# Performance work log

Measured on AMD Instinct MI355X. Metric: run time of the kernel, lower is better.

The kernel has to match this reference:

```python
import jax, jax.numpy as jnp
import numpy as np

B, N, G, K, C = 16, 8192, 128, 32, 384
EPS = 1e-5


def _fps(xyz, n):
    # furthest point sampling starting at index 0 (matches pointnet2 CUDA op)
    b = xyz.shape[0]
    dists = jnp.sum((xyz - xyz[:, :1]) ** 2, -1)  # [B,N] dist^2 to first pt

    def step(d, _):
        idx = jnp.argmax(d, axis=-1)                       # [B]
        p = jnp.take_along_axis(xyz, idx[:, None, None], 1)  # [B,1,3]
        d = jnp.minimum(d, jnp.sum((xyz - p) ** 2, -1))
        return d, idx.astype(jnp.int32)

    _, idxs = jax.lax.scan(step, dists, None, length=n - 1)
    idx = jnp.concatenate([jnp.zeros((1, b), jnp.int32), idxs], 0).T  # [B,n]
    return jnp.take_along_axis(xyz, idx[..., None], axis=1)


def _morton_order(center):
    # greedy nearest-neighbour tour over group centers (simplied_morton_sorting)
    b, g, _ = center.shape
    d = jnp.sum((center[:, :, None] - center[:, None]) ** 2, -1)  # [B,G,G]
    d = jnp.where(jnp.eye(g, dtype=bool), jnp.inf, d)

    def step(carry, _):
        cur, visited = carry
        row = jnp.take_along_axis(d, cur[:, None, None], 1)[:, 0]  # [B,G]
        row = jnp.where(visited, jnp.inf, row)
        nxt = jnp.argmin(row, -1).astype(jnp.int32)
        visited = visited | jax.nn.one_hot(nxt, g, dtype=bool)
        return (nxt, visited), nxt

    cur0 = jnp.zeros((b,), jnp.int32)
    init = (cur0, jax.nn.one_hot(cur0, g, dtype=bool))
    _, nxts = jax.lax.scan(step, init, None, length=g - 1)
    return jnp.concatenate([jnp.zeros((1, b), jnp.int32), nxts], 0).T  # [B,G]


def _bn(x, g_, b_, m_, v_):
    return (x - m_) * (g_ * jax.lax.rsqrt(v_ + EPS)) + b_


def _pos_embed(center):
    npf = 128  # 384 // 3 // 2 * 2
    i = jnp.arange(npf, dtype=jnp.float32)
    dim_t = 10000.0 ** (2.0 * jnp.floor(i / 2) / npf)
    x = center * (2.0 * np.pi)
    pd = x[..., None] / dim_t                                # [B,G,3,128]
    emb = jnp.stack([jnp.sin(pd[..., 0::2]), jnp.cos(pd[..., 1::2])], -1)
    return emb.reshape(*center.shape[:-1], -1)               # [B,G,384]


def _forward(xyz, w1, b1, g1, bt1, m1, v1, w2, b2, w3, b3, g3, bt3, m3, v3, w4, b4):
    center = _fps(xyz, G)                                    # [B,G,3]
    # squared-distance KNN (argsort order identical to euclidean cdist)
    d2 = (jnp.sum(center ** 2, -1)[:, :, None]
          + jnp.sum(xyz ** 2, -1)[:, None]
          - 2.0 * jnp.einsum('bgd,bnd->bgn', center, xyz))   # [B,G,N]
    _, idx = jax.lax.top_k(-d2, K)                           # [B,G,K]
    neigh = jnp.take_along_axis(xyz, idx.reshape(B, G * K)[..., None], 1)
    neigh = neigh.reshape(B, G, K, 3) - center[:, :, None]
    order = _morton_order(center)                            # [B,G]
    neigh = jnp.take_along_axis(neigh, order[:, :, None, None], 1)
    center = jnp.take_along_axis(center, order[:, :, None], 1)
    # Encoder_small (1x1 convs == per-point linears, eval-mode BN)
    pg = neigh.reshape(B * G, K, 3)
    f = jax.nn.relu(_bn(pg @ w1.T + b1, g1, bt1, m1, v1)) @ w2.T + b2  # [BG,K,256]
    fg = jnp.max(f, 1, keepdims=True)
    h = jnp.concatenate([jnp.broadcast_to(fg, f.shape), f], -1)        # [BG,K,512]
    h = jax.nn.relu(_bn(h @ w3.T + b3, g3, bt3, m3, v3)) @ w4.T + b4   # [BG,K,384]
    tokens = jnp.max(h, 1).reshape(B, G, C)
    return tokens + _pos_embed(center)


def setup_inputs() -> dict:
    key = jax.random.key(0)
    ks = jax.random.split(key, 8)
    s = 0.05
    return {
        'xyz': jax.random.normal(ks[0], (B, N, 3), jnp.float32),
        'w1': jax.random.normal(ks[1], (128, 3), jnp.float32) * s,
        'b1': jax.random.normal(ks[2], (128,), jnp.float32) * s,
        'g1': jnp.ones((128,), jnp.float32),
        'bt1': jnp.zeros((128,), jnp.float32),
        'm1': jnp.zeros((128,), jnp.float32),
        'v1': jnp.ones((128,), jnp.float32),
        'w2': jax.random.normal(ks[3], (256, 128), jnp.float32) * s,
        'b2': jax.random.normal(ks[4], (256,), jnp.float32) * s,
        'w3': jax.random.normal(ks[5], (512, 512), jnp.float32) * s,
        'b3': jnp.zeros((512,), jnp.float32),
        'g3': jnp.ones((512,), jnp.float32),
        'bt3': jnp.zeros((512,), jnp.float32),
        'm3': jnp.zeros((512,), jnp.float32),
        'v3': jnp.ones((512,), jnp.float32),
        'w4': jax.random.normal(ks[6], (384, 512), jnp.float32) * s,
        'b4': jax.random.normal(ks[7], (384,), jnp.float32) * s,
    }


def reference(xyz, w1, b1, g1, bt1, m1, v1, w2, b2, w3, b3, g3, bt3, m3, v3, w4, b4):
    return _forward(xyz, w1, b1, g1, bt1, m1, v1, w2, b2, w3, b3, g3, bt3, m3, v3, w4, b4)
```

## Files before the change

### kernel.cpp

```cpp
#include <hip/hip_runtime.h>
#include <hip/hip_bf16.h>

#define B_ 16
#define N_ 8192
#define G_ 128
#define K_ 32
#define C_ 384
#define EPSV 1e-5f

typedef __attribute__((ext_vector_type(8))) short bf16x8;
typedef __attribute__((ext_vector_type(8))) unsigned short u16x8;
typedef __attribute__((ext_vector_type(4))) float f32x4;
typedef __attribute__((ext_vector_type(2))) float f32x2;

__device__ __forceinline__ unsigned short f2b(float f){
  unsigned int u = __float_as_uint(f);
  u += 0x7fffu + ((u >> 16) & 1u);
  return (unsigned short)(u >> 16);
}
__device__ __forceinline__ float b2f(unsigned short s){
  return __uint_as_float(((unsigned int)s) << 16);
}
__device__ __forceinline__ float sq3(float dx, float dy, float dz){
  return __fadd_rn(__fadd_rn(__fmul_rn(dx,dx), __fmul_rn(dy,dy)), __fmul_rn(dz,dz));
}
__device__ __forceinline__ f32x2 pkmax(f32x2 a, f32x2 b){
  return f32x2{fmaxf(a.x,b.x), fmaxf(a.y,b.y)};
}
__device__ __forceinline__ unsigned fenc(float f){
  unsigned u = __float_as_uint(f);
  return ((int)u >= 0) ? (u | 0x80000000u) : ~u;
}

#define DPP_MAXU_STAGE(r, CTRL) { \
  unsigned _o = (unsigned)__builtin_amdgcn_update_dpp((int)(r), (int)(r), (CTRL), 0xf, 0xf, false); \
  (r) = ((r) > _o) ? (r) : _o; }
#define DPP_MAXU_ALL(r) \
  DPP_MAXU_STAGE(r, 0x111) DPP_MAXU_STAGE(r, 0x112) DPP_MAXU_STAGE(r, 0x114) \
  DPP_MAXU_STAGE(r, 0x118) DPP_MAXU_STAGE(r, 0x142) DPP_MAXU_STAGE(r, 0x143)
#define DPP_MINU_STAGE(r, CTRL) { \
  unsigned _o = (unsigned)__builtin_amdgcn_update_dpp((int)(r), (int)(r), (CTRL), 0xf, 0xf, false); \
  (r) = ((r) < _o) ? (r) : _o; }
#define DPP_MINU_ALL(r) \
  DPP_MINU_STAGE(r, 0x111) DPP_MINU_STAGE(r, 0x112) DPP_MINU_STAGE(r, 0x114) \
  DPP_MINU_STAGE(r, 0x118) DPP_MINU_STAGE(r, 0x142) DPP_MINU_STAGE(r, 0x143)

__global__ __launch_bounds__(256) void prep_kernel(
    const float* __restrict__ w2, const float* __restrict__ w3,
    const float* __restrict__ w4, unsigned short* __restrict__ w2b,
    unsigned short* __restrict__ w3b, unsigned short* __restrict__ w4b){
  int i = blockIdx.x*256 + threadIdx.x;
  if (i < 32768){ w2b[i] = f2b(w2[i]); return; }
  i -= 32768;
  if (i < 262144){ w3b[i] = f2b(w3[i]); return; }
  i -= 262144;
  if (i < 196608){ w4b[i] = f2b(w4[i]); }
}

__attribute__((amdgpu_flat_work_group_size(256,256), amdgpu_waves_per_eu(1,1)))
__global__ void fps_morton_kernel(const float* __restrict__ xyz,
                                  float* __restrict__ centers_ord){
  const int b = blockIdx.x, t = threadIdx.x, w = t >> 6;
  const int lane = t & 63;
  const float* xb = xyz + (size_t)b*N_*3;
  __shared__ __align__(16) float sval[2][4];
  __shared__ __align__(16) int   sidx[2][4];
  __shared__ float clx[G_], cly[G_], clz[G_];
  const int base = t*32;
  f32x2 X[16], Y[16], Z[16], D[16];
  const float p0x = xb[0], p0y = xb[1], p0z = xb[2];
  {
#pragma clang fp contract(off)
    float s[96];
    const float4* src = (const float4*)(xb + (size_t)base*3);
    #pragma unroll
    for (int q = 0; q < 24; q++) ((float4*)s)[q] = src[q];
    #pragma unroll
    for (int p = 0; p < 16; p++){
      X[p] = f32x2{s[6*p+0], s[6*p+3]};
      Y[p] = f32x2{s[6*p+1], s[6*p+4]};
      Z[p] = f32x2{s[6*p+2], s[6*p+5]};
      const f32x2 dx = X[p] - p0x, dy = Y[p] - p0y, dz = Z[p] - p0z;
      D[p] = (dx*dx + dy*dy) + dz*dz;
    }
  }
  if (t == 0){ clx[0] = p0x; cly[0] = p0y; clz[0] = p0z; }
  int buf = 0;
  for (int g = 1; g < G_; g++){
    const f32x2 mm = pkmax(pkmax(pkmax(pkmax(D[0],D[1]),pkmax(D[2],D[3])),
                                 pkmax(pkmax(D[4],D[5]),pkmax(D[6],D[7]))),
                           pkmax(pkmax(pkmax(D[8],D[9]),pkmax(D[10],D[11])),
                                 pkmax(pkmax(D[12],D[13]),pkmax(D[14],D[15]))));
    const float v = fmaxf(mm.x, mm.y);
    int jl = 0;
    #pragma unroll
    for (int p = 15; p >= 0; p--){
      if (D[p].y == v) jl = 2*p+1;
      if (D[p].x == v) jl = 2*p;
    }
    const unsigned uv = __float_as_uint(v);
    unsigned r = uv;
    DPP_MAXU_ALL(r)
    const unsigned wmax = (unsigned)__builtin_amdgcn_readlane((int)r, 63);
    const unsigned long long tie = __ballot(uv == wmax);
    const int wl = __ffsll(tie) - 1;
    if (lane == wl){ sval[buf][w] = __uint_as_float(wmax); sidx[buf][w] = base + jl; }
    __syncthreads();
    const float4 vv = *(const float4*)&sval[buf][0];
    const int4   ii = *(const int4*)&sidx[buf][0];
    float bv = vv.x; int bb = ii.x;
    if (vv.y > bv){ bv = vv.y; bb = ii.y; }
    if (vv.z > bv){ bv = vv.z; bb = ii.z; }
    if (vv.w > bv){ bv = vv.w; bb = ii.w; }
    {
#pragma clang fp contract(off)
      const int ubb = __builtin_amdgcn_readfirstlane(bb);
      const float cx = xb[ubb*3], cy = xb[ubb*3+1], cz = xb[ubb*3+2];
      if (t == 0){ clx[g] = cx; cly[g] = cy; clz[g] = cz; }
      #pragma unroll
      for (int p = 0; p < 16; p++){
        const f32x2 dx = X[p] - cx, dy = Y[p] - cy, dz = Z[p] - cz;
        const f32x2 dn = (dx*dx + dy*dy) + dz*dz;
        D[p] = f32x2{fminf(D[p].x, dn.x), fminf(D[p].y, dn.y)};
      }
    }
    buf ^= 1;
  }
  __syncthreads();
  if (t < 64){
    float mcx[2], mcy[2], mcz[2]; bool mvis[2];
    #pragma unroll
    for (int j = 0; j < 2; j++){
      const int idx = lane + j*64;
      mcx[j] = clx[idx]; mcy[j] = cly[idx]; mcz[j] = clz[idx];
      mvis[j] = (idx == 0);
    }
    float curx = clx[0], cury = cly[0], curz = clz[0];
    if (lane == 0){
      centers_ord[(size_t)b*G_*3 + 0] = curx;
      centers_ord[(size_t)b*G_*3 + 1] = cury;
      centers_ord[(size_t)b*G_*3 + 2] = curz;
    }
    for (int step = 1; step < G_; step++){
      const float d0r = sq3(__fsub_rn(mcx[0],curx), __fsub_rn(mcy[0],cury), __fsub_rn(mcz[0],curz));
      const float d1r = sq3(__fsub_rn(mcx[1],curx), __fsub_rn(mcy[1],cury), __fsub_rn(mcz[1],curz));
      const float d0 = mvis[0] ? __builtin_inff() : d0r;
      const float d1 = mvis[1] ? __builtin_inff() : d1r;
      float mv = d0; int mi = lane;
      if (d1 < mv){ mv = d1; mi = lane + 64; }
      const int wj = mi >> 6;
      const float sx = wj ? mcx[1] : mcx[0];
      const float sy = wj ? mcy[1] : mcy[0];
      const float sz = wj ? mcz[1] : mcz[0];
      const unsigned key = __float_as_uint(mv);
      unsigned r = key;
      DPP_MINU_ALL(r)
      const unsigned wmin = (unsigned)__builtin_amdgcn_readlane((int)r, 63);
      const unsigned long long tie = __ballot(key == wmin);
      int wl;
      if (__popcll(tie) == 1){
        wl = __ffsll(tie) - 1;
      } else {
        float tv = mv; int ti = mi;
        #pragma unroll
        for (int mk = 1; mk < 64; mk <<= 1){
          const float ov = __shfl_xor(tv, mk);
          const int   oi = __shfl_xor(ti, mk);
          if (ov < tv || (ov == tv && oi < ti)){ tv = ov; ti = oi; }
        }
        wl = ti & 63;
      }
      const int mbi = __builtin_amdgcn_readlane(mi, wl);
      curx = __uint_as_float((unsigned)__builtin_amdgcn_readlane((int)__float_as_uint(sx), wl));
      cury = __uint_as_float((unsigned)__builtin_amdgcn_readlane((int)__float_as_uint(sy), wl));
      curz = __uint_as_float((unsigned)__builtin_amdgcn_readlane((int)__float_as_uint(sz), wl));
      if (lane == wl){
        if ((mbi >> 6) == 0) mvis[0] = true; else mvis[1] = true;
      }
      if (lane == 0){
        centers_ord[((size_t)b*G_ + step)*3 + 0] = curx;
        centers_ord[((size_t)b*G_ + step)*3 + 1] = cury;
        centers_ord[((size_t)b*G_ + step)*3 + 2] = curz;
      }
    }
  }
}

__global__ __launch_bounds__(256, 2) void knn_kernel(const float* __restrict__ xyz,
                                                     const float* __restrict__ centers_ord,
                                                     float* __restrict__ neigh){
  const int gp = blockIdx.x, b = blockIdx.y, t = threadIdx.x;
  const int lane = t & 63, w = t >> 6;
  __shared__ __align__(16) float sv[2][4];
  __shared__ __align__(16) int   si[2][4];
  __shared__ int list[K_];
  const float* xb = xyz + (size_t)b*N_*3;
  const float* cp = centers_ord + ((size_t)b*G_ + gp)*3;
  const float cxv = cp[0], cyv = cp[1], czv = cp[2];
  const float cc = sq3(cxv, cyv, czv);
  const int base = t*32;
  float dd[32];
  float v = __builtin_inff(); int jl = 0;
  {
    float s[96];
    const float4* src = (const float4*)(xb + (size_t)base*3);
    #pragma unroll
    for (int q = 0; q < 24; q++) ((float4*)s)[q] = src[q];
    #pragma unroll
    for (int j = 0; j < 32; j++){
      const float x = s[3*j], y = s[3*j+1], z = s[3*j+2];
      const float xx = sq3(x, y, z);
      const float dot = __fadd_rn(__fadd_rn(__fmul_rn(cxv,x), __fmul_rn(cyv,y)), __fmul_rn(czv,z));
      dd[j] = __fsub_rn(__fadd_rn(cc, xx), __fmul_rn(2.f, dot));
      if (dd[j] < v){ v = dd[j]; jl = j; }
    }
  }
  int buf = 0;
  for (int it = 0; it < K_; it++){
    const unsigned key = fenc(v);
    unsigned r = key;
    DPP_MINU_ALL(r)
    const unsigned wmin = (unsigned)__builtin_amdgcn_readlane((int)r, 63);
    const unsigned long long tie = __ballot(key == wmin);
    const int wl = __ffsll(tie) - 1;
    if (lane == wl){ sv[buf][w] = v; si[buf][w] = base + jl; }
    __syncthreads();
    const float4 vv = *(const float4*)&sv[buf][0];
    const int4   ii = *(const int4*)&si[buf][0];
    float bv = vv.x; int bb = ii.x;
    if (vv.y < bv){ bv = vv.y; bb = ii.y; }
    if (vv.z < bv){ bv = vv.z; bb = ii.z; }
    if (vv.w < bv){ bv = vv.w; bb = ii.w; }
    if (t == 0) list[it] = bb;
    if ((bb >> 5) == t){
      const int jw = bb & 31;
      #pragma unroll
      for (int j = 0; j < 32; j++) if (j == jw) dd[j] = __builtin_inff();
      v = __builtin_inff(); jl = 0;
      #pragma unroll
      for (int j = 0; j < 32; j++) if (dd[j] < v){ v = dd[j]; jl = j; }
    }
    buf ^= 1;
  }
  __syncthreads();
  if (t < K_*3){
    const int k = t / 3, d = t % 3;
    const int n = list[k];
    neigh[(((size_t)b*G_ + gp)*K_ + k)*3 + d] = __fsub_rn(xb[n*3+d], cp[d]);
  }
}

__device__ __forceinline__ int swzA1(int row, int col){
  int byteo = row*256 + col*2;
  byteo ^= (row & 7) << 4;
  return byteo >> 1;
}
__device__ __forceinline__ int swzF(int row, int col){
  int byteo = row*512 + col*2;
  byteo ^= (row & 7) << 4;
  return byteo >> 1;
}
__device__ __forceinline__ int swzA(int row, int col){
  int byteo = row*1024 + col*2;
  byteo ^= (row & 7) << 4;
  return byteo >> 1;
}

__global__ __launch_bounds__(512, 2) void enc_kernel(
    const float* __restrict__ neigh, const float* __restrict__ centers_ord,
    const float* __restrict__ w1, const float* __restrict__ b1,
    const float* __restrict__ g1, const float* __restrict__ bt1,
    const float* __restrict__ m1, const float* __restrict__ v1,
    const unsigned short* __restrict__ w2b, const float* __restrict__ b2,
    const unsigned short* __restrict__ w3b, const float* __restrict__ b3,
    const float* __restrict__ g3, const float* __restrict__ bt3,
    const float* __restrict__ m3, const float* __restrict__ v3,
    const unsigned short* __restrict__ w4b, const float* __restrict__ b4,
    float* __restrict__ out)
{
  const int t = threadIdx.x;
  const int lane = t & 63, w = t >> 6, lr = lane & 15, lg = lane >> 4;
  const int gid0 = blockIdx.x*2;
  __shared__ __align__(16) unsigned short A1s[2][32*128];
  __shared__ __align__(16) unsigned short Fl[2][32*256];
  __shared__ __align__(16) unsigned short A3s[2][32*512];
  __shared__ __align__(16) unsigned short fgb[2][256];
  float* tokp = (float*)&Fl[0][0];

  {
    const int g = t >> 8, rem = t & 255, p = rem >> 3, c0 = (rem & 7) * 16;
    const float* pgp = neigh + (size_t)(gid0 + g)*96 + p*3;
    const float px = pgp[0], py = pgp[1], pz = pgp[2];
    unsigned short hv[16];
    #pragma unroll
    for (int cc = 0; cc < 16; cc++){
      const int c = c0 + cc;
      const float wx = w1[c*3], wy = w1[c*3+1], wz = w1[c*3+2];
      const float sc = g1[c] * rsqrtf(v1[c] + EPSV);
      float val = px*wx + py*wy + pz*wz + b1[c];
      val = (val - m1[c])*sc + bt1[c];
      hv[cc] = f2b(fmaxf(val, 0.f));
    }
    *(u16x8*)&A1s[g][swzA1(p, c0)]     = *(u16x8*)&hv[0];
    *(u16x8*)&A1s[g][swzA1(p, c0 + 8)] = *(u16x8*)&hv[8];
  }
  __syncthreads();

  {
    const int col0 = w*32;
    f32x4 acc[2][2][2];
    #pragma unroll
    for (int nt = 0; nt < 2; nt++)
      #pragma unroll
      for (int g = 0; g < 2; g++)
        #pragma unroll
        for (int m = 0; m < 2; m++){ f32x4 z = {0.f,0.f,0.f,0.f}; acc[nt][g][m] = z; }
    #pragma unroll
    for (int kt = 0; kt < 4; kt++){
      bf16x8 bA[2][2];
      #pragma unroll
      for (int g = 0; g < 2; g++)
        #pragma unroll
        for (int m = 0; m < 2; m++)
          bA[g][m] = *(const bf16x8*)&A1s[g][swzA1(m*16 + lr, kt*32 + lg*8)];
      bf16x8 bB[2];
      #pragma unroll
      for (int nt = 0; nt < 2; nt++)
        bB[nt] = *(const bf16x8*)(w2b + (size_t)(col0 + nt*16 + lr)*128 + kt*32 + lg*8);
      #pragma unroll
      for (int nt = 0; nt < 2; nt++)
        #pragma unroll
        for (int g = 0; g < 2; g++)
          #pragma unroll
          for (int m = 0; m < 2; m++)
            acc[nt][g][m] = __builtin_amdgcn_mfma_f32_16x16x32_bf16(bA[g][m], bB[nt], acc[nt][g][m], 0,0,0);
    }
    #pragma unroll
    for (int nt = 0; nt < 2; nt++){
      const int col = col0 + nt*16 + lr;
      const float bc = b2[col];
      #pragma unroll
      for (int g = 0; g < 2; g++)
        #pragma unroll
        for (int m = 0; m < 2; m++)
          #pragma unroll
          for (int r = 0; r < 4; r++)
            Fl[g][swzF(m*16 + lg*4 + r, col)] = f2b(acc[nt][g][m][r] + bc);
    }
  }
  __syncthreads();

  {
    const int g = t >> 8, col = t & 255;
    float mx = -__builtin_inff();
    #pragma unroll 4
    for (int row = 0; row < 32; row++) mx = fmaxf(mx, b2f(Fl[g][swzF(row, col)]));
    fgb[g][col] = f2b(mx);
  }
  __syncthreads();

  {
    const int col0 = w*64;
    f32x4 acc[4][2][2];
    #pragma unroll
    for (int nt = 0; nt < 4; nt++)
      #pragma unroll
      for (int g = 0; g < 2; g++)
        #pragma unroll
        for (int m = 0; m < 2; m++){ f32x4 z = {0.f,0.f,0.f,0.f}; acc[nt][g][m] = z; }
    #pragma unroll
    for (int kt = 0; kt < 16; kt++){
      bf16x8 bA[2][2];
      if (kt < 8){
        #pragma unroll
        for (int g = 0; g < 2; g++){
          const bf16x8 af = *(const bf16x8*)&fgb[g][kt*32 + lg*8];
          bA[g][0] = af; bA[g][1] = af;
        }
      } else {
        #pragma unroll
        for (int g = 0; g < 2; g++)
          #pragma unroll
          for (int m = 0; m < 2; m++)
            bA[g][m] = *(const bf16x8*)&Fl[g][swzF(m*16 + lr, (kt-8)*32 + lg*8)];
      }
      bf16x8 bB[4];
      #pragma unroll
      for (int nt = 0; nt < 4; nt++)
        bB[nt] = *(const bf16x8*)(w3b + (size_t)(col0 + nt*16 + lr)*512 + kt*32 + lg*8);
      #pragma unroll
      for (int nt = 0; nt < 4; nt++)
        #pragma unroll
        for (int g = 0; g < 2; g++)
          #pragma unroll
          for (int m = 0; m < 2; m++)
            acc[nt][g][m] = __builtin_amdgcn_mfma_f32_16x16x32_bf16(bA[g][m], bB[nt], acc[nt][g][m], 0,0,0);
    }
    #pragma unroll
    for (int nt = 0; nt < 4; nt++){
      const int col = col0 + nt*16 + lr;
      const float bc = b3[col];
      const float sc = g3[col]*rsqrtf(v3[col] + EPSV);
      const float mm = m3[col], bb = bt3[col];
      #pragma unroll
      for (int g = 0; g < 2; g++)
        #pragma unroll
        for (int m = 0; m < 2; m++)
          #pragma unroll
          for (int r = 0; r < 4; r++){
            float val = acc[nt][g][m][r] + bc;
            val = (val - mm)*sc + bb;
            A3s[g][swzA(m*16 + lg*4 + r, col)] = f2b(fmaxf(val, 0.f));
          }
    }
  }
  __syncthreads();

  {
    const int col0 = w*48;
    f32x4 acc[3][2][2];
    #pragma unroll
    for (int nt = 0; nt < 3; nt++)
      #pragma unroll
      for (int g = 0; g < 2; g++)
        #pragma unroll
        for (int m = 0; m < 2; m++){ f32x4 z = {0.f,0.f,0.f,0.f}; acc[nt][g][m] = z; }
    #pragma unroll
    for (int kt = 0; kt < 16; kt++){
      bf16x8 bA[2][2];
      #pragma unroll
      for (int g = 0; g < 2; g++)
        #pragma unroll
        for (int m = 0; m < 2; m++)
          bA[g][m] = *(const bf16x8*)&A3s[g][swzA(m*16 + lr, kt*32 + lg*8)];
      bf16x8 bB[3];
      #pragma unroll
      for (int nt = 0; nt < 3; nt++)
        bB[nt] = *(const bf16x8*)(w4b + (size_t)(col0 + nt*16 + lr)*512 + kt*32 + lg*8);
      #pragma unroll
      for (int nt = 0; nt < 3; nt++)
        #pragma unroll
        for (int g = 0; g < 2; g++)
          #pragma unroll
          for (int m = 0; m < 2; m++)
            acc[nt][g][m] = __builtin_amdgcn_mfma_f32_16x16x32_bf16(bA[g][m], bB[nt], acc[nt][g][m], 0,0,0);
    }
    #pragma unroll
    for (int nt = 0; nt < 3; nt++){
      const int col = col0 + nt*16 + lr;
      const float bc = b4[col];
      #pragma unroll
      for (int g = 0; g < 2; g++){
        float mx = fmaxf(
          fmaxf(fmaxf(acc[nt][g][0][0], acc[nt][g][0][1]), fmaxf(acc[nt][g][0][2], acc[nt][g][0][3])),
          fmaxf(fmaxf(acc[nt][g][1][0], acc[nt][g][1][1]), fmaxf(acc[nt][g][1][2], acc[nt][g][1][3])));
        mx = fmaxf(mx, __shfl_xor(mx, 16));
        mx = fmaxf(mx, __shfl_xor(mx, 32));
        if (lg == 0) tokp[g*C_ + col] = mx + bc;
      }
    }
  }
  __syncthreads();

  for (int c2 = t; c2 < 2*C_; c2 += 512){
    const int g = (c2 >= C_) ? 1 : 0;
    const int c = c2 - g*C_;
    const int gid = gid0 + g;
    const int d = c >> 7, r = c & 127, m2 = r >> 1;
    const float e = (float)(2*m2) * (1.f/128.f);
    const float dimt = powf(10000.f, e);
    const float ctrd = centers_ord[(size_t)gid*3 + d];
    const float x2 = __fmul_rn(ctrd, 6.28318530717958647692f);
    const float ang = __fdiv_rn(x2, dimt);
    out[(size_t)gid*C_ + c] = tokp[g*C_ + c] + ((r & 1) ? cosf(ang) : sinf(ang));
  }
}

extern "C" void kernel_launch(void* const* d_in, const int* in_sizes, int n_in,
                              void* d_out, int out_size, void* d_ws, size_t ws_size,
                              hipStream_t stream){
  (void)in_sizes; (void)n_in; (void)out_size; (void)ws_size;
  const float* xyz = (const float*)d_in[0];
  const float* w1  = (const float*)d_in[1];
  const float* b1  = (const float*)d_in[2];
  const float* g1  = (const float*)d_in[3];
  const float* bt1 = (const float*)d_in[4];
  const float* m1  = (const float*)d_in[5];
  const float* v1  = (const float*)d_in[6];
  const float* w2  = (const float*)d_in[7];
  const float* b2  = (const float*)d_in[8];
  const float* w3  = (const float*)d_in[9];
  const float* b3  = (const float*)d_in[10];
  const float* g3  = (const float*)d_in[11];
  const float* bt3 = (const float*)d_in[12];
  const float* m3  = (const float*)d_in[13];
  const float* v3  = (const float*)d_in[14];
  const float* w4  = (const float*)d_in[15];
  const float* b4  = (const float*)d_in[16];

  char* ws = (char*)d_ws;
  float* centers_ord  = (float*)(ws + 24576);
  float* neigh        = (float*)(ws + 49152);
  unsigned short* w2b = (unsigned short*)(ws + 835584);
  unsigned short* w3b = (unsigned short*)(ws + 901120);
  unsigned short* w4b = (unsigned short*)(ws + 1425408);

  prep_kernel      <<<1920, 256, 0, stream>>>(w2, w3, w4, w2b, w3b, w4b);
  fps_morton_kernel<<<B_, 256, 0, stream>>>(xyz, centers_ord);
  knn_kernel       <<<dim3(G_, B_), 256, 0, stream>>>(xyz, centers_ord, neigh);
  enc_kernel       <<<1024, 512, 0, stream>>>(neigh, centers_ord,
      w1, b1, g1, bt1, m1, v1, w2b, b2, w3b, b3, g3, bt3, m3, v3, w4b, b4,
      (float*)d_out);
}
```

Measured before the change: 511.2 us.

## Fold FPS running max into distance update; encode three groups per block

In the FPS loop, the per-thread maximum is now updated while each new minimum distance is written, so the separate 16-way max tree before the selection step goes away. The encoder kernel now handles three point groups per block instead of two, so each weight fragment loaded from global memory feeds more MFMAs. To make room, it uses one aliased shared-memory buffer of about 149 KB, and the grid shrinks to 683 blocks. The larger LDS footprint probably allows only one block per CU. The last block still computes a padded third group, reading neighbour data just past the valid range, but it writes no output for it.

```diff
diff --git a/kernel.cpp b/kernel.cpp
--- a/kernel.cpp
+++ b/kernel.cpp
@@ -68,6 +68,7 @@
   __shared__ float clx[G_], cly[G_], clz[G_];
   const int base = t*32;
   f32x2 X[16], Y[16], Z[16], D[16];
+  f32x2 mmax;
   const float p0x = xb[0], p0y = xb[1], p0z = xb[2];
   {
 #pragma clang fp contract(off)
@@ -75,6 +76,7 @@
     const float4* src = (const float4*)(xb + (size_t)base*3);
     #pragma unroll
     for (int q = 0; q < 24; q++) ((float4*)s)[q] = src[q];
+    mmax = f32x2{-1.f, -1.f};
     #pragma unroll
     for (int p = 0; p < 16; p++){
       X[p] = f32x2{s[6*p+0], s[6*p+3]};
@@ -82,16 +84,13 @@
       Z[p] = f32x2{s[6*p+2], s[6*p+5]};
       const f32x2 dx = X[p] - p0x, dy = Y[p] - p0y, dz = Z[p] - p0z;
       D[p] = (dx*dx + dy*dy) + dz*dz;
+      mmax = pkmax(mmax, D[p]);
     }
   }
   if (t == 0){ clx[0] = p0x; cly[0] = p0y; clz[0] = p0z; }
   int buf = 0;
   for (int g = 1; g < G_; g++){
-    const f32x2 mm = pkmax(pkmax(pkmax(pkmax(D[0],D[1]),pkmax(D[2],D[3])),
-                                 pkmax(pkmax(D[4],D[5]),pkmax(D[6],D[7]))),
-                           pkmax(pkmax(pkmax(D[8],D[9]),pkmax(D[10],D[11])),
-                                 pkmax(pkmax(D[12],D[13]),pkmax(D[14],D[15]))));
-    const float v = fmaxf(mm.x, mm.y);
+    const float v = fmaxf(mmax.x, mmax.y);
     int jl = 0;
     #pragma unroll
     for (int p = 15; p >= 0; p--){
@@ -117,11 +116,13 @@
       const int ubb = __builtin_amdgcn_readfirstlane(bb);
       const float cx = xb[ubb*3], cy = xb[ubb*3+1], cz = xb[ubb*3+2];
       if (t == 0){ clx[g] = cx; cly[g] = cy; clz[g] = cz; }
+      mmax = f32x2{-1.f, -1.f};
       #pragma unroll
       for (int p = 0; p < 16; p++){
         const f32x2 dx = X[p] - cx, dy = Y[p] - cy, dz = Z[p] - cz;
         const f32x2 dn = (dx*dx + dy*dy) + dz*dz;
         D[p] = f32x2{fminf(D[p].x, dn.x), fminf(D[p].y, dn.y)};
+        mmax = pkmax(mmax, D[p]);
       }
     }
     buf ^= 1;
@@ -266,6 +267,8 @@
   return byteo >> 1;
 }
 
+#define NG3 3
+
 __global__ __launch_bounds__(512, 2) void enc_kernel(
     const float* __restrict__ neigh, const float* __restrict__ centers_ord,
     const float* __restrict__ w1, const float* __restrict__ b1,
@@ -280,15 +283,17 @@
 {
   const int t = threadIdx.x;
   const int lane = t & 63, w = t >> 6, lr = lane & 15, lg = lane >> 4;
-  const int gid0 = blockIdx.x*2;
-  __shared__ __align__(16) unsigned short A1s[2][32*128];
-  __shared__ __align__(16) unsigned short Fl[2][32*256];
-  __shared__ __align__(16) unsigned short A3s[2][32*512];
-  __shared__ __align__(16) unsigned short fgb[2][256];
-  float* tokp = (float*)&Fl[0][0];
-
-  {
-    const int g = t >> 8, rem = t & 255, p = rem >> 3, c0 = (rem & 7) * 16;
+  const int gid0 = blockIdx.x*NG3;
+  const int ng = min(NG3, 2048 - gid0);
+  __shared__ __align__(16) char smem[148992];
+  unsigned short* A3s = (unsigned short*)smem;
+  unsigned short* A1s = (unsigned short*)smem;
+  unsigned short* Flp = (unsigned short*)(smem + 98304);
+  unsigned short* fgb = (unsigned short*)(smem + 147456);
+  float* tokp = (float*)(smem + 98304);
+
+  for (int it = t; it < NG3*256; it += 512){
+    const int g = it >> 8, rem = it & 255, p = rem >> 3, c0 = (rem & 7) * 16;
     const float* pgp = neigh + (size_t)(gid0 + g)*96 + p*3;
     const float px = pgp[0], py = pgp[1], pz = pgp[2];
     unsigned short hv[16];
@@ -301,28 +306,28 @@
       val = (val - m1[c])*sc + bt1[c];
       hv[cc] = f2b(fmaxf(val, 0.f));
     }
-    *(u16x8*)&A1s[g][swzA1(p, c0)]     = *(u16x8*)&hv[0];
-    *(u16x8*)&A1s[g][swzA1(p, c0 + 8)] = *(u16x8*)&hv[8];
+    *(u16x8*)&A1s[g*4096 + swzA1(p, c0)]     = *(u16x8*)&hv[0];
+    *(u16x8*)&A1s[g*4096 + swzA1(p, c0 + 8)] = *(u16x8*)&hv[8];
   }
   __syncthreads();
 
   {
     const int col0 = w*32;
-    f32x4 acc[2][2][2];
+    f32x4 acc[2][NG3][2];
     #pragma unroll
     for (int nt = 0; nt < 2; nt++)
       #pragma unroll
-      for (int g = 0; g < 2; g++)
+      for (int g = 0; g < NG3; g++)
         #pragma unroll
         for (int m = 0; m < 2; m++){ f32x4 z = {0.f,0.f,0.f,0.f}; acc[nt][g][m] = z; }
     #pragma unroll
     for (int kt = 0; kt < 4; kt++){
-      bf16x8 bA[2][2];
-      #pragma unroll
-      for (int g = 0; g < 2; g++)
+      bf16x8 bA[NG3][2];
+      #pragma unroll
+      for (int g = 0; g < NG3; g++)
         #pragma unroll
         for (int m = 0; m < 2; m++)
-          bA[g][m] = *(const bf16x8*)&A1s[g][swzA1(m*16 + lr, kt*32 + lg*8)];
+          bA[g][m] = *(const bf16x8*)&A1s[g*4096 + swzA1(m*16 + lr, kt*32 + lg*8)];
       bf16x8 bB[2];
       #pragma unroll
       for (int nt = 0; nt < 2; nt++)
@@ -330,7 +335,7 @@
       #pragma unroll
       for (int nt = 0; nt < 2; nt++)
         #pragma unroll
-        for (int g = 0; g < 2; g++)
+        for (int g = 0; g < NG3; g++)
           #pragma unroll
           for (int m = 0; m < 2; m++)
             acc[nt][g][m] = __builtin_amdgcn_mfma_f32_16x16x32_bf16(bA[g][m], bB[nt], acc[nt][g][m], 0,0,0);
@@ -340,49 +345,49 @@
       const int col = col0 + nt*16 + lr;
       const float bc = b2[col];
       #pragma unroll
-      for (int g = 0; g < 2; g++)
+      for (int g = 0; g < NG3; g++)
         #pragma unroll
         for (int m = 0; m < 2; m++)
           #pragma unroll
           for (int r = 0; r < 4; r++)
-            Fl[g][swzF(m*16 + lg*4 + r, col)] = f2b(acc[nt][g][m][r] + bc);
-    }
-  }
-  __syncthreads();
-
-  {
-    const int g = t >> 8, col = t & 255;
+            Flp[g*8192 + swzF(m*16 + lg*4 + r, col)] = f2b(acc[nt][g][m][r] + bc);
+    }
+  }
+  __syncthreads();
+
+  for (int it = t; it < NG3*256; it += 512){
+    const int g = it >> 8, col = it & 255;
     float mx = -__builtin_inff();
     #pragma unroll 4
-    for (int row = 0; row < 32; row++) mx = fmaxf(mx, b2f(Fl[g][swzF(row, col)]));
-    fgb[g][col] = f2b(mx);
+    for (int row = 0; row < 32; row++) mx = fmaxf(mx, b2f(Flp[g*8192 + swzF(row, col)]));
+    fgb[g*256 + col] = f2b(mx);
   }
   __syncthreads();
 
   {
     const int col0 = w*64;
-    f32x4 acc[4][2][2];
+    f32x4 acc[4][NG3][2];
     #pragma unroll
     for (int nt = 0; nt < 4; nt++)
       #pragma unroll
-      for (int g = 0; g < 2; g++)
+      for (int g = 0; g < NG3; g++)
         #pragma unroll
         for (int m = 0; m < 2; m++){ f32x4 z = {0.f,0.f,0.f,0.f}; acc[nt][g][m] = z; }
     #pragma unroll
     for (int kt = 0; kt < 16; kt++){
-      bf16x8 bA[2][2];
+      bf16x8 bA[NG3][2];
       if (kt < 8){
         #pragma unroll
-        for (int g = 0; g < 2; g++){
-          const bf16x8 af = *(const bf16x8*)&fgb[g][kt*32 + lg*8];
+        for (int g = 0; g < NG3; g++){
+          const bf16x8 af = *(const bf16x8*)&fgb[g*256 + kt*32 + lg*8];
           bA[g][0] = af; bA[g][1] = af;
         }
       } else {
         #pragma unroll
-        for (int g = 0; g < 2; g++)
+        for (int g = 0; g < NG3; g++)
           #pragma unroll
           for (int m = 0; m < 2; m++)
-            bA[g][m] = *(const bf16x8*)&Fl[g][swzF(m*16 + lr, (kt-8)*32 + lg*8)];
+            bA[g][m] = *(const bf16x8*)&Flp[g*8192 + swzF(m*16 + lr, (kt-8)*32 + lg*8)];
       }
       bf16x8 bB[4];
       #pragma unroll
@@ -391,7 +396,7 @@
       #pragma unroll
       for (int nt = 0; nt < 4; nt++)
         #pragma unroll
-        for (int g = 0; g < 2; g++)
+        for (int g = 0; g < NG3; g++)
           #pragma unroll
           for (int m = 0; m < 2; m++)
             acc[nt][g][m] = __builtin_amdgcn_mfma_f32_16x16x32_bf16(bA[g][m], bB[nt], acc[nt][g][m], 0,0,0);
@@ -403,14 +408,14 @@
       const float sc = g3[col]*rsqrtf(v3[col] + EPSV);
       const float mm = m3[col], bb = bt3[col];
       #pragma unroll
-      for (int g = 0; g < 2; g++)
+      for (int g = 0; g < NG3; g++)
         #pragma unroll
         for (int m = 0; m < 2; m++)
           #pragma unroll
           for (int r = 0; r < 4; r++){
             float val = acc[nt][g][m][r] + bc;
             val = (val - mm)*sc + bb;
-            A3s[g][swzA(m*16 + lg*4 + r, col)] = f2b(fmaxf(val, 0.f));
+            A3s[g*16384 + swzA(m*16 + lg*4 + r, col)] = f2b(fmaxf(val, 0.f));
           }
     }
   }
@@ -418,21 +423,21 @@
 
   {
     const int col0 = w*48;
-    f32x4 acc[3][2][2];
+    f32x4 acc[3][NG3][2];
     #pragma unroll
     for (int nt = 0; nt < 3; nt++)
       #pragma unroll
-      for (int g = 0; g < 2; g++)
+      for (int g = 0; g < NG3; g++)
         #pragma unroll
         for (int m = 0; m < 2; m++){ f32x4 z = {0.f,0.f,0.f,0.f}; acc[nt][g][m] = z; }
     #pragma unroll
     for (int kt = 0; kt < 16; kt++){
-      bf16x8 bA[2][2];
-      #pragma unroll
-      for (int g = 0; g < 2; g++)
+      bf16x8 bA[NG3][2];
+      #pragma unroll
+      for (int g = 0; g < NG3; g++)
         #pragma unroll
         for (int m = 0; m < 2; m++)
-          bA[g][m] = *(const bf16x8*)&A3s[g][swzA(m*16 + lr, kt*32 + lg*8)];
+          bA[g][m] = *(const bf16x8*)&A3s[g*16384 + swzA(m*16 + lr, kt*32 + lg*8)];
       bf16x8 bB[3];
       #pragma unroll
       for (int nt = 0; nt < 3; nt++)
@@ -440,7 +445,7 @@
       #pragma unroll
       for (int nt = 0; nt < 3; nt++)
         #pragma unroll
-        for (int g = 0; g < 2; g++)
+        for (int g = 0; g < NG3; g++)
           #pragma unroll
           for (int m = 0; m < 2; m++)
             acc[nt][g][m] = __builtin_amdgcn_mfma_f32_16x16x32_bf16(bA[g][m], bB[nt], acc[nt][g][m], 0,0,0);
@@ -450,7 +455,7 @@
       const int col = col0 + nt*16 + lr;
       const float bc = b4[col];
       #pragma unroll
-      for (int g = 0; g < 2; g++){
+      for (int g = 0; g < NG3; g++){
         float mx = fmaxf(
           fmaxf(fmaxf(acc[nt][g][0][0], acc[nt][g][0][1]), fmaxf(acc[nt][g][0][2], acc[nt][g][0][3])),
           fmaxf(fmaxf(acc[nt][g][1][0], acc[nt][g][1][1]), fmaxf(acc[nt][g][1][2], acc[nt][g][1][3])));
@@ -462,17 +467,19 @@
   }
   __syncthreads();
 
-  for (int c2 = t; c2 < 2*C_; c2 += 512){
-    const int g = (c2 >= C_) ? 1 : 0;
-    const int c = c2 - g*C_;
+  #pragma unroll
+  for (int g = 0; g < NG3; g++){
+    if (g >= ng) break;
     const int gid = gid0 + g;
-    const int d = c >> 7, r = c & 127, m2 = r >> 1;
-    const float e = (float)(2*m2) * (1.f/128.f);
-    const float dimt = powf(10000.f, e);
-    const float ctrd = centers_ord[(size_t)gid*3 + d];
-    const float x2 = __fmul_rn(ctrd, 6.28318530717958647692f);
-    const float ang = __fdiv_rn(x2, dimt);
-    out[(size_t)gid*C_ + c] = tokp[g*C_ + c] + ((r & 1) ? cosf(ang) : sinf(ang));
+    for (int c = t; c < C_; c += 512){
+      const int d = c >> 7, r = c & 127, m2 = r >> 1;
+      const float e = (float)(2*m2) * (1.f/128.f);
+      const float dimt = powf(10000.f, e);
+      const float ctrd = centers_ord[(size_t)gid*3 + d];
+      const float x2 = __fmul_rn(ctrd, 6.28318530717958647692f);
+      const float ang = __fdiv_rn(x2, dimt);
+      out[(size_t)gid*C_ + c] = tokp[g*C_ + c] + ((r & 1) ? cosf(ang) : sinf(ang));
+    }
   }
 }
 
@@ -508,7 +515,7 @@
   prep_kernel      <<<1920, 256, 0, stream>>>(w2, w3, w4, w2b, w3b, w4b);
   fps_morton_kernel<<<B_, 256, 0, stream>>>(xyz, centers_ord);
   knn_kernel       <<<dim3(G_, B_), 256, 0, stream>>>(xyz, centers_ord, neigh);
-  enc_kernel       <<<1024, 512, 0, stream>>>(neigh, centers_ord,
+  enc_kernel       <<<683, 512, 0, stream>>>(neigh, centers_ord,
       w1, b1, g1, bt1, m1, v1, w2b, b2, w3b, b3, g3, bt3, m3, v3, w4b, b4,
       (float*)d_out);
 }
```

Measured after the change: 478.4 us. 6.4% less time.
